# Performance work log

Measured on AMD Instinct MI355X. Metric: run time of the kernel, lower is better.

The kernel has to match this reference:

```python
import jax, jax.numpy as jnp
import numpy as np

DIM = 1024
HEADS = 16
DIM_HEAD = 64
INNER = HEADS * DIM_HEAD  # 1024
EPS = 1e-5


def layer_norm(x, g, b):
    mu = jnp.mean(x, axis=-1, keepdims=True)
    var = jnp.var(x, axis=-1, keepdims=True)
    return (x - mu) * jax.lax.rsqrt(var + EPS) * g + b


def setup_inputs() -> dict:
    key = jax.random.key(0)
    ks = jax.random.split(key, 8)
    s = 0.02
    return {
        "x": jax.random.normal(ks[0], (2, 2048, DIM), dtype=jnp.float32),
        "w_qkv": jax.random.normal(ks[1], (DIM, 3 * INNER), dtype=jnp.float32) * s,
        "w_out": jax.random.normal(ks[2], (INNER, DIM), dtype=jnp.float32) * s,
        "b_out": jnp.zeros((DIM,), jnp.float32),
        "g1": jnp.ones((DIM,), jnp.float32),
        "bt1": jnp.zeros((DIM,), jnp.float32),
        "g2": jnp.ones((DIM,), jnp.float32),
        "bt2": jnp.zeros((DIM,), jnp.float32),
        "w1": jax.random.normal(ks[3], (DIM, DIM), dtype=jnp.float32) * s,  # ff hidden = dim_out = DIM
        "b1": jnp.zeros((DIM,), jnp.float32),
        "w2": jax.random.normal(ks[4], (DIM, DIM), dtype=jnp.float32) * s,
        "b2": jnp.zeros((DIM,), jnp.float32),
    }


def reference(x, w_qkv, w_out, b_out, g1, bt1, g2, bt2, w1, b1, w2, b2):
    b, n, _ = x.shape
    scale = DIM_HEAD ** (-0.5)
    x_in = x
    xl = layer_norm(x, g1, bt1)
    qkv = xl @ w_qkv  # [b, n, 3*inner]
    q, k, v = jnp.split(qkv, 3, axis=-1)
    def split_heads(t):
        return t.reshape(b, n, HEADS, DIM_HEAD).transpose(0, 2, 1, 3)  # b h n d
    q, k, v = map(split_heads, (q, k, v))
    dots = jnp.einsum('bhid,bhjd->bhij', q, k) * scale
    attn = jax.nn.softmax(dots, axis=-1)
    out = jnp.einsum('bhij,bhjd->bhid', attn, v)
    out = out.transpose(0, 2, 1, 3).reshape(b, n, INNER)
    out = out @ w_out + b_out
    out = out + x_in
    h = layer_norm(out, g2, bt2)
    h = jax.nn.gelu(h @ w1 + b1, approximate=False) @ w2 + b2
    return h + out
```

## Files before the change

kernel.cpp:

```cpp
#include <hip/hip_runtime.h>
#include <math.h>

typedef __attribute__((ext_vector_type(4))) float f32x4;
typedef __attribute__((ext_vector_type(8))) short bf16x8;
typedef __attribute__((ext_vector_type(8))) unsigned short u16x8;

#define DIM 1024
#define SEQ 2048
#define NHEADS 16
#define DH 64

__device__ __forceinline__ unsigned short f2bf(float f) {
    unsigned int u = __builtin_bit_cast(unsigned int, f);
    u += 0x7fffu + ((u >> 16) & 1u);
    return (unsigned short)(u >> 16);
}

__device__ __forceinline__ float bf2f(unsigned short s) {
    unsigned int u = (unsigned int)s << 16;
    return __builtin_bit_cast(float, u);
}

__device__ __forceinline__ unsigned int cvt_pk_bf16(float lo, float hi) {
    unsigned int r;
    asm("v_cvt_pk_bf16_f32 %0, %1, %2" : "=v"(r) : "v"(lo), "v"(hi));
    return r;
}

__device__ __forceinline__ float fexp2(float x) {
    float r;
    asm("v_exp_f32 %0, %1" : "=v"(r) : "v"(x));
    return r;
}

__device__ __forceinline__ void gld16(const unsigned short* g, unsigned short* l) {
    __builtin_amdgcn_global_load_lds((const __attribute__((address_space(1))) void*)g,
                                     (__attribute__((address_space(3))) void*)l, 16, 0, 0);
}

__global__ __launch_bounds__(256) void wtrans_ln(const float* __restrict__ wq,
                                                 const float* __restrict__ wo,
                                                 const float* __restrict__ wf1,
                                                 const float* __restrict__ wf2,
                                                 unsigned short* __restrict__ oq,
                                                 unsigned short* __restrict__ oo,
                                                 unsigned short* __restrict__ of1,
                                                 unsigned short* __restrict__ of2, float sc,
                                                 const float* __restrict__ x,
                                                 const float* __restrict__ g1,
                                                 const float* __restrict__ bt1,
                                                 unsigned short* __restrict__ xl) {
    int z = blockIdx.z;
    int bxi = blockIdx.x;
    int tid = threadIdx.x;
    if (z == 4) {
        int row = blockIdx.y * 128 + bxi;
        const float4* xr = (const float4*)(x + (size_t)row * DIM);
        float4 v = xr[tid];
        float s1 = v.x + v.y + v.z + v.w;
        float s2 = v.x * v.x + v.y * v.y + v.z * v.z + v.w * v.w;
#pragma unroll
        for (int m = 32; m >= 1; m >>= 1) {
            s1 += __shfl_xor(s1, m);
            s2 += __shfl_xor(s2, m);
        }
        __shared__ float r1[4], r2[4];
        int w = tid >> 6;
        if ((tid & 63) == 0) { r1[w] = s1; r2[w] = s2; }
        __syncthreads();
        s1 = r1[0] + r1[1] + r1[2] + r1[3];
        s2 = r2[0] + r2[1] + r2[2] + r2[3];
        float mu = s1 * (1.0f / DIM);
        float var = s2 * (1.0f / DIM) - mu * mu;
        float rstd = rsqrtf(var + 1e-5f);
        float4 g4 = ((const float4*)g1)[tid];
        float4 b4 = ((const float4*)bt1)[tid];
        ushort4 ov;
        ov.x = f2bf((v.x - mu) * rstd * g4.x + b4.x);
        ov.y = f2bf((v.y - mu) * rstd * g4.y + b4.y);
        ov.z = f2bf((v.z - mu) * rstd * g4.z + b4.z);
        ov.w = f2bf((v.w - mu) * rstd * g4.w + b4.w);
        *(ushort4*)(xl + (size_t)row * DIM + tid * 4) = ov;
        return;
    }
    if (bxi >= (z == 0 ? 96 : 32)) return;
    const float* w = z == 0 ? wq : z == 1 ? wo : z == 2 ? wf1 : wf2;
    unsigned short* wt = z == 0 ? oq : z == 1 ? oo : z == 2 ? of1 : of2;
    int N = z == 0 ? 3072 : 1024;
    int scale_n = z == 0 ? 1024 : 0;
    const int K = 1024;
    __shared__ float t[32][33];
    int n0 = bxi * 32, k0 = blockIdx.y * 32;
    int c = tid & 31, rb = tid >> 5;
#pragma unroll
    for (int i = 0; i < 4; ++i) {
        int r = rb + i * 8;
        t[r][c] = w[(size_t)(k0 + r) * N + n0 + c];
    }
    __syncthreads();
#pragma unroll
    for (int i = 0; i < 4; ++i) {
        int r = rb + i * 8;
        float v = t[c][r];
        if (n0 + r < scale_n) v *= sc;
        wt[(size_t)(n0 + r) * K + k0 + c] = f2bf(v);
    }
}

__global__ __launch_bounds__(256) void ln_bf16(const unsigned short* __restrict__ x,
                                               const float* __restrict__ g,
                                               const float* __restrict__ bt,
                                               unsigned short* __restrict__ o) {
    int row = blockIdx.x, tid = threadIdx.x;
    ushort4 v4 = *(const ushort4*)(x + (size_t)row * DIM + tid * 4);
    float vx = bf2f(v4.x), vy = bf2f(v4.y), vz = bf2f(v4.z), vw = bf2f(v4.w);
    float s1 = vx + vy + vz + vw;
    float s2 = vx * vx + vy * vy + vz * vz + vw * vw;
#pragma unroll
    for (int m = 32; m >= 1; m >>= 1) {
        s1 += __shfl_xor(s1, m);
        s2 += __shfl_xor(s2, m);
    }
    __shared__ float r1[4], r2[4];
    int w = tid >> 6;
    if ((tid & 63) == 0) { r1[w] = s1; r2[w] = s2; }
    __syncthreads();
    s1 = r1[0] + r1[1] + r1[2] + r1[3];
    s2 = r2[0] + r2[1] + r2[2] + r2[3];
    float mu = s1 * (1.0f / DIM);
    float var = s2 * (1.0f / DIM) - mu * mu;
    float rstd = rsqrtf(var + 1e-5f);
    float4 g4 = ((const float4*)g)[tid];
    float4 b4 = ((const float4*)bt)[tid];
    ushort4 ov;
    ov.x = f2bf((vx - mu) * rstd * g4.x + b4.x);
    ov.y = f2bf((vy - mu) * rstd * g4.y + b4.y);
    ov.z = f2bf((vz - mu) * rstd * g4.z + b4.z);
    ov.w = f2bf((vw - mu) * rstd * g4.w + b4.w);
    *(ushort4*)(o + (size_t)row * DIM + tid * 4) = ov;
}

__global__ __launch_bounds__(512) void gemm256_qkv(const unsigned short* __restrict__ A,
                                                   const unsigned short* __restrict__ BT,
                                                   unsigned short* __restrict__ C,
                                                   unsigned short* __restrict__ vt,
                                                   int M, int N, int K, int nbx) {
    __shared__ unsigned short SM[65536];
    unsigned short* As = SM;
    unsigned short* Bs = SM + 32768;
    int tid = threadIdx.x;
    int lane = tid & 63, w = tid >> 6;
    int l15 = lane & 15, lhi = lane >> 4;
    int wr = w >> 2, wc = w & 3;
    int nwg = gridDim.x, wg = blockIdx.x;
    int swz = (wg & 7) * (nwg >> 3) + (wg >> 3);
    int bx = swz % nbx, by = swz / nbx;
    int row0 = by * 256, col0 = bx * 256;
    f32x4 zero = {0.f, 0.f, 0.f, 0.f};
    f32x4 acc[8][4];
#pragma unroll
    for (int i = 0; i < 8; ++i)
#pragma unroll
        for (int j = 0; j < 4; ++j) acc[i][j] = zero;
    auto stageA = [&](int slot, int kt) {
#pragma unroll
        for (int p = 0; p < 4; ++p) {
            int u = tid + p * 512;
            int r = u >> 3, cu = u & 7;
            int scu = cu ^ (r & 7);
            gld16(A + (size_t)(row0 + r) * K + kt * 64 + scu * 8, As + slot * 16384 + u * 8);
        }
    };
    auto stageB = [&](int slot, int kt) {
#pragma unroll
        for (int p = 0; p < 4; ++p) {
            int u = tid + p * 512;
            int r = u >> 3, cu = u & 7;
            int scu = cu ^ (r & 7);
            gld16(BT + (size_t)(col0 + r) * K + kt * 64 + scu * 8, Bs + slot * 16384 + u * 8);
        }
    };
    int nk = K / 64;
    stageB(0, 0);
    stageA(0, 0);
    stageB(1, 1);
    stageA(1, 1);
    asm volatile("s_waitcnt vmcnt(8)" ::: "memory");
    __builtin_amdgcn_s_barrier();
    __builtin_amdgcn_sched_barrier(0);
    for (int t = 0; t < nk; ++t) {
        int cur = t & 1;
        const unsigned short* Ab = As + cur * 16384;
        const unsigned short* Bb = Bs + cur * 16384;
        bf16x8 bfr[4][2];
#pragma unroll
        for (int j = 0; j < 4; ++j)
#pragma unroll
            for (int kk = 0; kk < 2; ++kk) {
                int rr = wc * 64 + j * 16 + l15;
                bfr[j][kk] = *(const bf16x8*)&Bb[rr * 64 + (((kk * 4 + lhi) ^ (rr & 7)) * 8)];
            }
#pragma unroll
        for (int q = 0; q < 4; ++q) {
            bf16x8 af[2][2];
#pragma unroll
            for (int i2 = 0; i2 < 2; ++i2)
#pragma unroll
                for (int kk = 0; kk < 2; ++kk) {
                    int rr = wr * 128 + (q * 2 + i2) * 16 + l15;
                    af[i2][kk] = *(const bf16x8*)&Ab[rr * 64 + (((kk * 4 + lhi) ^ (rr & 7)) * 8)];
                }
#pragma unroll
            for (int kk = 0; kk < 2; ++kk)
#pragma unroll
                for (int i2 = 0; i2 < 2; ++i2)
#pragma unroll
                    for (int j = 0; j < 4; ++j)
                        acc[q * 2 + i2][j] = __builtin_amdgcn_mfma_f32_16x16x32_bf16(
                            af[i2][kk], bfr[j][kk], acc[q * 2 + i2][j], 0, 0, 0);
            if (q == 0) {
                __builtin_amdgcn_sched_barrier(0);
                __builtin_amdgcn_s_barrier();
                __builtin_amdgcn_sched_barrier(0);
                if (t + 2 < nk) stageB(cur, t + 2);
            }
        }
        __builtin_amdgcn_sched_barrier(0);
        __builtin_amdgcn_s_barrier();
        __builtin_amdgcn_sched_barrier(0);
        if (t + 2 < nk) stageA(cur, t + 2);
        if (t + 1 < nk) {
            if (t + 2 < nk)
                asm volatile("s_waitcnt vmcnt(8)" ::: "memory");
            else
                asm volatile("s_waitcnt vmcnt(0)" ::: "memory");
            __builtin_amdgcn_s_barrier();
            __builtin_amdgcn_sched_barrier(0);
        }
    }
    if (col0 >= 2048) {
        __builtin_amdgcn_sched_barrier(0);
        __syncthreads();
        unsigned short* Ct = SM;
#pragma unroll
        for (int i = 0; i < 8; ++i)
#pragma unroll
            for (int j = 0; j < 4; ++j)
#pragma unroll
                for (int r = 0; r < 4; ++r) {
                    int row = wr * 128 + i * 16 + lhi * 4 + r;
                    int col = wc * 64 + j * 16 + l15;
                    Ct[row * 256 + (col ^ (((row >> 2) & 7) << 3))] = f2bf(acc[i][j][r]);
                }
        __syncthreads();
        int b = row0 >> 11, n0 = row0 & 2047;
        int h0 = (col0 - 2048) >> 6;
        int c = tid >> 1, hf = tid & 1;
        int hl = c >> 6, d = c & 63;
        unsigned short* vrow =
            vt + ((size_t)(b * NHEADS + h0 + hl) * DH + d) * SEQ + n0 + hf * 128;
#pragma unroll
        for (int s8 = 0; s8 < 16; ++s8) {
            u16x8 val;
#pragma unroll
            for (int j = 0; j < 8; ++j) {
                int nn = hf * 128 + s8 * 8 + j;
                int ntl = nn >> 6, s = nn & 63;
                int sig = (s & 32) | ((s & 4) << 2) | ((s & 24) >> 1) | (s & 3);
                int rr = ntl * 64 + sig;
                val[j] = Ct[rr * 256 + (c ^ (((rr >> 2) & 7) << 3))];
            }
            *(u16x8*)(vrow + s8 * 8) = val;
        }
        return;
    }
#pragma unroll
    for (int i = 0; i < 8; ++i)
#pragma unroll
        for (int j = 0; j < 4; ++j)
#pragma unroll
            for (int r = 0; r < 4; ++r) {
                int row = row0 + wr * 128 + i * 16 + lhi * 4 + r;
                int col = col0 + wc * 64 + j * 16 + l15;
                C[(size_t)row * N + col] = f2bf(acc[i][j][r]);
            }
}

template <int BN, int BK, int OBF, int BIAS, int GELU_, int RESID>
__global__ __launch_bounds__(256) void gemm_kernel(const unsigned short* __restrict__ A,
                                                   const unsigned short* __restrict__ BT,
                                                   void* __restrict__ C,
                                                   const float* __restrict__ bias,
                                                   const void* __restrict__ resid,
                                                   int M, int N, int K, int nbx) {
    constexpr int U = BK / 8;
    constexpr int NAU = 128 * U;
    constexpr int NBU = BN * U;
    constexpr int PT = (NAU + NBU) / 256;
    constexpr int NJ = BN / 32;
    constexpr int KK = BK / 32;
    extern __shared__ char smem[];
    unsigned short* As = (unsigned short*)smem;
    unsigned short* Bs = As + 3 * 128 * BK;
    int tid = threadIdx.x;
    int lane = tid & 63, w = tid >> 6;
    int l15 = lane & 15, lhi = lane >> 4;
    int nwg = gridDim.x, wg = blockIdx.x;
    int swz = (wg & 7) * (nwg >> 3) + (wg >> 3);
    int bx = swz % nbx, by = swz / nbx;
    int row0 = by * 128, col0 = bx * BN;
    int wrow = (w >> 1) * 64, wcol = (w & 1) * (16 * NJ);
    auto rh = [](int rr) -> int {
        if constexpr (U == 4) return (rr ^ (rr >> 2)) & 3;
        else return rr & (U - 1);
    };
    f32x4 zero = {0.f, 0.f, 0.f, 0.f};
    f32x4 acc[4][NJ];
#pragma unroll
    for (int i = 0; i < 4; ++i)
#pragma unroll
        for (int j = 0; j < NJ; ++j) acc[i][j] = zero;
    auto stage = [&](int buf, int kt) {
#pragma unroll
        for (int p = 0; p < PT; ++p) {
            if (p * 256 < NAU) {
                int u = tid + p * 256;
                int r = u / U, cu = u % U;
                int scu = cu ^ rh(r);
                gld16(A + (size_t)(row0 + r) * K + kt * BK + scu * 8, As + buf * 128 * BK + u * 8);
            } else {
                int ub = tid + p * 256 - NAU;
                int r = ub / U, cu = ub % U;
                int scu = cu ^ rh(r);
                gld16(BT + (size_t)(col0 + r) * K + kt * BK + scu * 8, Bs + buf * BN * BK + ub * 8);
            }
        }
    };
    int nk = K / BK;
    stage(0, 0);
    stage(1, 1);
    asm volatile("s_waitcnt vmcnt(%0)" ::"i"(PT) : "memory");
    __builtin_amdgcn_s_barrier();
    __builtin_amdgcn_sched_barrier(0);
    int cur = 0;
    for (int kt = 0; kt < nk; ++kt) {
        int nxt2 = cur + 2 >= 3 ? cur - 1 : cur + 2;
        if (kt + 2 < nk) stage(nxt2, kt + 2);
        const unsigned short* Ab = As + cur * 128 * BK;
        const unsigned short* Bb = Bs + cur * BN * BK;
        bf16x8 af[4][KK], bfr[NJ][KK];
#pragma unroll
        for (int i = 0; i < 4; ++i)
#pragma unroll
            for (int kk = 0; kk < KK; ++kk) {
                int rr = wrow + i * 16 + l15;
                int up = (kk * 4 + lhi) ^ rh(rr);
                af[i][kk] = *(const bf16x8*)&Ab[rr * BK + up * 8];
            }
#pragma unroll
        for (int j = 0; j < NJ; ++j)
#pragma unroll
            for (int kk = 0; kk < KK; ++kk) {
                int rr = wcol + j * 16 + l15;
                int up = (kk * 4 + lhi) ^ rh(rr);
                bfr[j][kk] = *(const bf16x8*)&Bb[rr * BK + up * 8];
            }
#pragma unroll
        for (int kk = 0; kk < KK; ++kk)
#pragma unroll
            for (int i = 0; i < 4; ++i)
#pragma unroll
                for (int j = 0; j < NJ; ++j)
                    acc[i][j] = __builtin_amdgcn_mfma_f32_16x16x32_bf16(af[i][kk], bfr[j][kk],
                                                                        acc[i][j], 0, 0, 0);
        __builtin_amdgcn_sched_barrier(0);
        if (kt + 1 < nk) {
            if (kt + 2 < nk)
                asm volatile("s_waitcnt vmcnt(%0)" ::"i"(PT) : "memory");
            else
                asm volatile("s_waitcnt vmcnt(0)" ::: "memory");
            __builtin_amdgcn_s_barrier();
            __builtin_amdgcn_sched_barrier(0);
        }
        cur = cur + 1 == 3 ? 0 : cur + 1;
    }
#pragma unroll
    for (int i = 0; i < 4; ++i)
#pragma unroll
        for (int j = 0; j < NJ; ++j)
#pragma unroll
            for (int r = 0; r < 4; ++r) {
                int row = row0 + wrow + i * 16 + lhi * 4 + r;
                int col = col0 + wcol + j * 16 + l15;
                float v = acc[i][j][r];
                if (BIAS) v += bias[col];
                if (GELU_) v = 0.5f * v * (1.0f + erff(v * 0.70710678118f));
                if (RESID == 1) v += ((const float*)resid)[(size_t)row * N + col];
                if (RESID == 2) v += bf2f(((const unsigned short*)resid)[(size_t)row * N + col]);
                if (OBF)
                    ((unsigned short*)C)[(size_t)row * N + col] = f2bf(v);
                else
                    ((float*)C)[(size_t)row * N + col] = v;
            }
}

__global__ __launch_bounds__(256) void attn_kernel(const unsigned short* __restrict__ qkv,
                                                   const unsigned short* __restrict__ vt,
                                                   unsigned short* __restrict__ o) {
    __shared__ unsigned short Ks[2][64 * 64];
    __shared__ unsigned short Vs[2][64 * 64];
    int tid = threadIdx.x;
    int lane = tid & 63, w = tid >> 6;
    int l15 = lane & 15, lhi = lane >> 4;
    int wg = blockIdx.x;
    int swz = (wg & 7) * 128 + (wg >> 3);
    int qt = swz & 31, h = (swz >> 5) & 15, b = swz >> 9;
    const unsigned short* qb =
        qkv + (size_t)(b * SEQ + qt * 64 + w * 16 + l15) * 3072 + h * DH;
    bf16x8 qf0 = *(const bf16x8*)(qb + lhi * 8);
    bf16x8 qf1 = *(const bf16x8*)(qb + 32 + lhi * 8);
    f32x4 zero = {0.f, 0.f, 0.f, 0.f};
    f32x4 oacc[4], lacc = zero;
#pragma unroll
    for (int i = 0; i < 4; ++i) oacc[i] = zero;
    const short one_s = (short)0x3F80;
    bf16x8 ones = {one_s, one_s, one_s, one_s, one_s, one_s, one_s, one_s};
    int srow = tid >> 3;
    int scx = (tid & 7) ^ (srow & 7);
    const unsigned short* kb = qkv + (size_t)b * SEQ * 3072 + 1024 + h * DH;
    const unsigned short* vb = vt + (size_t)(b * NHEADS + h) * DH * SEQ;
    const unsigned short* k0 = kb + (size_t)srow * 3072 + scx * 8;
    const unsigned short* v0 = vb + (size_t)srow * SEQ + scx * 8;
    auto stage = [&](int buf, int kt) {
        unsigned short* lk = &Ks[buf][0] + tid * 8;
        unsigned short* lv = &Vs[buf][0] + tid * 8;
        gld16(k0 + (size_t)kt * 64 * 3072, lk);
        gld16(k0 + ((size_t)kt * 64 + 32) * 3072, lk + 2048);
        gld16(v0 + kt * 64, lv);
        gld16(v0 + (size_t)32 * SEQ + kt * 64, lv + 2048);
    };
    const int NT = SEQ / 64;
    stage(0, 0);
    asm volatile("s_waitcnt vmcnt(0)" ::: "memory");
    __builtin_amdgcn_s_barrier();
    __builtin_amdgcn_sched_barrier(0);
    int kx = l15 & 7;
    for (int kt = 0; kt < NT; ++kt) {
        int cur = kt & 1;
        if (kt + 1 < NT) stage(cur ^ 1, kt + 1);
        const unsigned short* Kc = &Ks[cur][0];
        const unsigned short* Vc = &Vs[cur][0];
        f32x4 sacc[4];
#pragma unroll
        for (int nt = 0; nt < 4; ++nt) {
            bf16x8 kf0 = *(const bf16x8*)&Kc[(nt * 16 + l15) * 64 + ((lhi ^ kx) * 8)];
            bf16x8 kf1 = *(const bf16x8*)&Kc[(nt * 16 + l15) * 64 + (((4 + lhi) ^ kx) * 8)];
            f32x4 z = __builtin_amdgcn_mfma_f32_16x16x32_bf16(kf0, qf0, zero, 0, 0, 0);
            sacc[nt] = __builtin_amdgcn_mfma_f32_16x16x32_bf16(kf1, qf1, z, 0, 0, 0);
        }
        bf16x8 pf[2];
#pragma unroll
        for (int kc = 0; kc < 2; ++kc) {
            union { bf16x8 v; unsigned int u[4]; } pu;
            pu.u[0] = cvt_pk_bf16(fexp2(sacc[2 * kc][0]), fexp2(sacc[2 * kc][1]));
            pu.u[1] = cvt_pk_bf16(fexp2(sacc[2 * kc][2]), fexp2(sacc[2 * kc][3]));
            pu.u[2] = cvt_pk_bf16(fexp2(sacc[2 * kc + 1][0]), fexp2(sacc[2 * kc + 1][1]));
            pu.u[3] = cvt_pk_bf16(fexp2(sacc[2 * kc + 1][2]), fexp2(sacc[2 * kc + 1][3]));
            pf[kc] = pu.v;
        }
#pragma unroll
        for (int dt = 0; dt < 4; ++dt)
#pragma unroll
            for (int kc = 0; kc < 2; ++kc) {
                bf16x8 vf = *(const bf16x8*)&Vc[(dt * 16 + l15) * 64 + (((kc * 4 + lhi) ^ kx) * 8)];
                oacc[dt] = __builtin_amdgcn_mfma_f32_16x16x32_bf16(vf, pf[kc], oacc[dt], 0, 0, 0);
            }
        lacc = __builtin_amdgcn_mfma_f32_16x16x32_bf16(ones, pf[0], lacc, 0, 0, 0);
        lacc = __builtin_amdgcn_mfma_f32_16x16x32_bf16(ones, pf[1], lacc, 0, 0, 0);
        __builtin_amdgcn_sched_barrier(0);
        if (kt + 1 < NT) {
            asm volatile("s_waitcnt vmcnt(0)" ::: "memory");
            __builtin_amdgcn_s_barrier();
            __builtin_amdgcn_sched_barrier(0);
        }
    }
    float rl = 1.0f / lacc[0];
    size_t orow = (size_t)(b * SEQ + qt * 64 + w * 16 + l15) * DIM + h * DH;
#pragma unroll
    for (int dt = 0; dt < 4; ++dt) {
        ushort4 st;
        st.x = f2bf(oacc[dt][0] * rl);
        st.y = f2bf(oacc[dt][1] * rl);
        st.z = f2bf(oacc[dt][2] * rl);
        st.w = f2bf(oacc[dt][3] * rl);
        *(ushort4*)(o + orow + dt * 16 + lhi * 4) = st;
    }
}

extern "C" void kernel_launch(void* const* d_in, const int* in_sizes, int n_in,
                              void* d_out, int out_size, void* d_ws, size_t ws_size,
                              hipStream_t stream) {
    (void)in_sizes; (void)n_in; (void)out_size; (void)ws_size;
    const float* x = (const float*)d_in[0];
    const float* w_qkv = (const float*)d_in[1];
    const float* w_out = (const float*)d_in[2];
    const float* b_out = (const float*)d_in[3];
    const float* g1 = (const float*)d_in[4];
    const float* bt1 = (const float*)d_in[5];
    const float* g2 = (const float*)d_in[6];
    const float* bt2 = (const float*)d_in[7];
    const float* w1 = (const float*)d_in[8];
    const float* b1 = (const float*)d_in[9];
    const float* w2 = (const float*)d_in[10];
    const float* b2 = (const float*)d_in[11];
    float* out = (float*)d_out;

    char* ws = (char*)d_ws;
    size_t off = 0;
    auto alloc = [&](size_t bytes) {
        void* p = ws + off;
        off += (bytes + 255) & ~(size_t)255;
        return p;
    };
    const int R = 2 * SEQ;
    unsigned short* xl    = (unsigned short*)alloc((size_t)R * DIM * 2);
    unsigned short* wqkvT = (unsigned short*)alloc((size_t)3 * DIM * DIM * 2);
    unsigned short* woutT = (unsigned short*)alloc((size_t)DIM * DIM * 2);
    unsigned short* w1T   = (unsigned short*)alloc((size_t)DIM * DIM * 2);
    unsigned short* w2T   = (unsigned short*)alloc((size_t)DIM * DIM * 2);
    unsigned short* qkvb  = (unsigned short*)alloc((size_t)R * 3 * DIM * 2);
    unsigned short* vtb   = (unsigned short*)alloc((size_t)R * DIM * 2);
    unsigned short* attO  = (unsigned short*)alloc((size_t)R * DIM * 2);
    unsigned short* outb  = (unsigned short*)alloc((size_t)R * DIM * 2);
    unsigned short* h2    = (unsigned short*)alloc((size_t)R * DIM * 2);
    unsigned short* ffn1  = (unsigned short*)alloc((size_t)R * DIM * 2);

    const float CS = 0.125f * 1.44269504f;
    wtrans_ln<<<dim3(128, 32, 5), 256, 0, stream>>>(w_qkv, w_out, w1, w2, wqkvT, woutT, w1T, w2T,
                                                    CS, x, g1, bt1, xl);

    const unsigned int SH_FFN = (3 * 128 * 64 + 3 * 64 * 64) * 2;
    gemm256_qkv<<<dim3((R / 256) * (3 * DIM / 256)), 512, 0, stream>>>(
        xl, wqkvT, qkvb, vtb, R, 3 * DIM, DIM, 3 * DIM / 256);
    attn_kernel<<<2 * NHEADS * (SEQ / 64), 256, 0, stream>>>(qkvb, vtb, attO);
    gemm_kernel<64, 64, 1, 1, 0, 1><<<dim3((DIM / 64) * (R / 128)), 256, SH_FFN, stream>>>(
        attO, woutT, outb, b_out, x, R, DIM, DIM, DIM / 64);
    ln_bf16<<<R, 256, 0, stream>>>(outb, g2, bt2, h2);
    gemm_kernel<64, 64, 1, 1, 1, 0><<<dim3((DIM / 64) * (R / 128)), 256, SH_FFN, stream>>>(
        h2, w1T, ffn1, b1, nullptr, R, DIM, DIM, DIM / 64);
    gemm_kernel<64, 64, 0, 1, 0, 2><<<dim3((DIM / 64) * (R / 128)), 256, SH_FFN, stream>>>(
        ffn1, w2T, out, b2, outb, R, DIM, DIM, DIM / 64);
}
```

Before: 155.3 us.

## Split attention over KV quarters with 128-row Q tiles and add combine kernel

The attention kernel now handles 128 query rows per block, two 16-row groups per wave, so each K/V tile in shared memory is reused twice as often. The key sequence is split into four quarters across separate blocks (split-K), each writing unnormalized bf16 partial outputs and row sums, and a new combine kernel adds the partials and normalizes. Double buffering of K/V is dropped in favour of a single buffer with load, wait, then compute. The change trades more grid parallelism and fewer LDS loads per MFMA for extra global traffic on partial outputs, an extra launch, bf16 rounding of partials and no load/compute overlap.

```diff
diff --git a/kernel.cpp b/kernel.cpp
--- a/kernel.cpp
+++ b/kernel.cpp
@@ -406,23 +406,32 @@
 
 __global__ __launch_bounds__(256) void attn_kernel(const unsigned short* __restrict__ qkv,
                                                    const unsigned short* __restrict__ vt,
-                                                   unsigned short* __restrict__ o) {
-    __shared__ unsigned short Ks[2][64 * 64];
-    __shared__ unsigned short Vs[2][64 * 64];
+                                                   unsigned short* __restrict__ po,
+                                                   float* __restrict__ pl) {
+    __shared__ unsigned short Ks[64 * 64];
+    __shared__ unsigned short Vs[64 * 64];
     int tid = threadIdx.x;
     int lane = tid & 63, w = tid >> 6;
     int l15 = lane & 15, lhi = lane >> 4;
     int wg = blockIdx.x;
-    int swz = (wg & 7) * 128 + (wg >> 3);
-    int qt = swz & 31, h = (swz >> 5) & 15, b = swz >> 9;
-    const unsigned short* qb =
-        qkv + (size_t)(b * SEQ + qt * 64 + w * 16 + l15) * 3072 + h * DH;
-    bf16x8 qf0 = *(const bf16x8*)(qb + lhi * 8);
-    bf16x8 qf1 = *(const bf16x8*)(qb + 32 + lhi * 8);
+    int swz = (wg & 7) * 256 + (wg >> 3);
+    int qt = swz & 15, quarter = (swz >> 4) & 3, h = (swz >> 6) & 15, b = swz >> 10;
+    bf16x8 qf[2][2];
+#pragma unroll
+    for (int qg = 0; qg < 2; ++qg) {
+        const unsigned short* qb =
+            qkv + (size_t)(b * SEQ + qt * 128 + w * 32 + qg * 16 + l15) * 3072 + h * DH;
+        qf[qg][0] = *(const bf16x8*)(qb + lhi * 8);
+        qf[qg][1] = *(const bf16x8*)(qb + 32 + lhi * 8);
+    }
     f32x4 zero = {0.f, 0.f, 0.f, 0.f};
-    f32x4 oacc[4], lacc = zero;
-#pragma unroll
-    for (int i = 0; i < 4; ++i) oacc[i] = zero;
+    f32x4 oacc[2][4], lacc[2];
+#pragma unroll
+    for (int qg = 0; qg < 2; ++qg) {
+        lacc[qg] = zero;
+#pragma unroll
+        for (int i = 0; i < 4; ++i) oacc[qg][i] = zero;
+    }
     const short one_s = (short)0x3F80;
     bf16x8 ones = {one_s, one_s, one_s, one_s, one_s, one_s, one_s, one_s};
     int srow = tid >> 3;
@@ -431,70 +440,104 @@
     const unsigned short* vb = vt + (size_t)(b * NHEADS + h) * DH * SEQ;
     const unsigned short* k0 = kb + (size_t)srow * 3072 + scx * 8;
     const unsigned short* v0 = vb + (size_t)srow * SEQ + scx * 8;
-    auto stage = [&](int buf, int kt) {
-        unsigned short* lk = &Ks[buf][0] + tid * 8;
-        unsigned short* lv = &Vs[buf][0] + tid * 8;
-        gld16(k0 + (size_t)kt * 64 * 3072, lk);
-        gld16(k0 + ((size_t)kt * 64 + 32) * 3072, lk + 2048);
-        gld16(v0 + kt * 64, lv);
-        gld16(v0 + (size_t)32 * SEQ + kt * 64, lv + 2048);
+    auto stage = [&](int kg) {
+        unsigned short* lk = &Ks[0] + tid * 8;
+        unsigned short* lv = &Vs[0] + tid * 8;
+        gld16(k0 + (size_t)kg * 64 * 3072, lk);
+        gld16(k0 + ((size_t)kg * 64 + 32) * 3072, lk + 2048);
+        gld16(v0 + kg * 64, lv);
+        gld16(v0 + (size_t)32 * SEQ + kg * 64, lv + 2048);
     };
-    const int NT = SEQ / 64;
-    stage(0, 0);
-    asm volatile("s_waitcnt vmcnt(0)" ::: "memory");
-    __builtin_amdgcn_s_barrier();
-    __builtin_amdgcn_sched_barrier(0);
     int kx = l15 & 7;
-    for (int kt = 0; kt < NT; ++kt) {
-        int cur = kt & 1;
-        if (kt + 1 < NT) stage(cur ^ 1, kt + 1);
-        const unsigned short* Kc = &Ks[cur][0];
-        const unsigned short* Vc = &Vs[cur][0];
-        f32x4 sacc[4];
+    const int NT4 = SEQ / 64 / 4;
+    for (int kt = 0; kt < NT4; ++kt) {
+        stage(quarter * NT4 + kt);
+        asm volatile("s_waitcnt vmcnt(0)" ::: "memory");
+        __builtin_amdgcn_s_barrier();
+        __builtin_amdgcn_sched_barrier(0);
+        f32x4 sacc[2][4];
 #pragma unroll
         for (int nt = 0; nt < 4; ++nt) {
-            bf16x8 kf0 = *(const bf16x8*)&Kc[(nt * 16 + l15) * 64 + ((lhi ^ kx) * 8)];
-            bf16x8 kf1 = *(const bf16x8*)&Kc[(nt * 16 + l15) * 64 + (((4 + lhi) ^ kx) * 8)];
-            f32x4 z = __builtin_amdgcn_mfma_f32_16x16x32_bf16(kf0, qf0, zero, 0, 0, 0);
-            sacc[nt] = __builtin_amdgcn_mfma_f32_16x16x32_bf16(kf1, qf1, z, 0, 0, 0);
-        }
-        bf16x8 pf[2];
-#pragma unroll
-        for (int kc = 0; kc < 2; ++kc) {
-            union { bf16x8 v; unsigned int u[4]; } pu;
-            pu.u[0] = cvt_pk_bf16(fexp2(sacc[2 * kc][0]), fexp2(sacc[2 * kc][1]));
-            pu.u[1] = cvt_pk_bf16(fexp2(sacc[2 * kc][2]), fexp2(sacc[2 * kc][3]));
-            pu.u[2] = cvt_pk_bf16(fexp2(sacc[2 * kc + 1][0]), fexp2(sacc[2 * kc + 1][1]));
-            pu.u[3] = cvt_pk_bf16(fexp2(sacc[2 * kc + 1][2]), fexp2(sacc[2 * kc + 1][3]));
-            pf[kc] = pu.v;
-        }
+            bf16x8 kf0 = *(const bf16x8*)&Ks[(nt * 16 + l15) * 64 + ((lhi ^ kx) * 8)];
+            bf16x8 kf1 = *(const bf16x8*)&Ks[(nt * 16 + l15) * 64 + (((4 + lhi) ^ kx) * 8)];
+#pragma unroll
+            for (int qg = 0; qg < 2; ++qg) {
+                f32x4 z = __builtin_amdgcn_mfma_f32_16x16x32_bf16(kf0, qf[qg][0], zero, 0, 0, 0);
+                sacc[qg][nt] = __builtin_amdgcn_mfma_f32_16x16x32_bf16(kf1, qf[qg][1], z, 0, 0, 0);
+            }
+        }
+        bf16x8 pf[2][2];
+#pragma unroll
+        for (int qg = 0; qg < 2; ++qg)
+#pragma unroll
+            for (int kc = 0; kc < 2; ++kc) {
+                union { bf16x8 v; unsigned int u[4]; } pu;
+                pu.u[0] = cvt_pk_bf16(fexp2(sacc[qg][2 * kc][0]), fexp2(sacc[qg][2 * kc][1]));
+                pu.u[1] = cvt_pk_bf16(fexp2(sacc[qg][2 * kc][2]), fexp2(sacc[qg][2 * kc][3]));
+                pu.u[2] = cvt_pk_bf16(fexp2(sacc[qg][2 * kc + 1][0]), fexp2(sacc[qg][2 * kc + 1][1]));
+                pu.u[3] = cvt_pk_bf16(fexp2(sacc[qg][2 * kc + 1][2]), fexp2(sacc[qg][2 * kc + 1][3]));
+                pf[qg][kc] = pu.v;
+            }
 #pragma unroll
         for (int dt = 0; dt < 4; ++dt)
 #pragma unroll
             for (int kc = 0; kc < 2; ++kc) {
-                bf16x8 vf = *(const bf16x8*)&Vc[(dt * 16 + l15) * 64 + (((kc * 4 + lhi) ^ kx) * 8)];
-                oacc[dt] = __builtin_amdgcn_mfma_f32_16x16x32_bf16(vf, pf[kc], oacc[dt], 0, 0, 0);
-            }
-        lacc = __builtin_amdgcn_mfma_f32_16x16x32_bf16(ones, pf[0], lacc, 0, 0, 0);
-        lacc = __builtin_amdgcn_mfma_f32_16x16x32_bf16(ones, pf[1], lacc, 0, 0, 0);
+                bf16x8 vf = *(const bf16x8*)&Vs[(dt * 16 + l15) * 64 + (((kc * 4 + lhi) ^ kx) * 8)];
+#pragma unroll
+                for (int qg = 0; qg < 2; ++qg)
+                    oacc[qg][dt] =
+                        __builtin_amdgcn_mfma_f32_16x16x32_bf16(vf, pf[qg][kc], oacc[qg][dt], 0, 0, 0);
+            }
+#pragma unroll
+        for (int qg = 0; qg < 2; ++qg) {
+            lacc[qg] = __builtin_amdgcn_mfma_f32_16x16x32_bf16(ones, pf[qg][0], lacc[qg], 0, 0, 0);
+            lacc[qg] = __builtin_amdgcn_mfma_f32_16x16x32_bf16(ones, pf[qg][1], lacc[qg], 0, 0, 0);
+        }
         __builtin_amdgcn_sched_barrier(0);
-        if (kt + 1 < NT) {
-            asm volatile("s_waitcnt vmcnt(0)" ::: "memory");
+        if (kt + 1 < NT4) {
             __builtin_amdgcn_s_barrier();
             __builtin_amdgcn_sched_barrier(0);
         }
     }
-    float rl = 1.0f / lacc[0];
-    size_t orow = (size_t)(b * SEQ + qt * 64 + w * 16 + l15) * DIM + h * DH;
-#pragma unroll
-    for (int dt = 0; dt < 4; ++dt) {
-        ushort4 st;
-        st.x = f2bf(oacc[dt][0] * rl);
-        st.y = f2bf(oacc[dt][1] * rl);
-        st.z = f2bf(oacc[dt][2] * rl);
-        st.w = f2bf(oacc[dt][3] * rl);
-        *(ushort4*)(o + orow + dt * 16 + lhi * 4) = st;
-    }
+#pragma unroll
+    for (int qg = 0; qg < 2; ++qg) {
+        int rrow = b * SEQ + qt * 128 + w * 32 + qg * 16 + l15;
+        unsigned short* pob = po + ((size_t)quarter * 4096 + rrow) * DIM + h * DH;
+#pragma unroll
+        for (int dt = 0; dt < 4; ++dt) {
+            ushort4 st;
+            st.x = f2bf(oacc[qg][dt][0]);
+            st.y = f2bf(oacc[qg][dt][1]);
+            st.z = f2bf(oacc[qg][dt][2]);
+            st.w = f2bf(oacc[qg][dt][3]);
+            *(ushort4*)(pob + dt * 16 + lhi * 4) = st;
+        }
+        if (lhi == 0) pl[((size_t)quarter * 4096 + rrow) * NHEADS + h] = lacc[qg][0];
+    }
+}
+
+__global__ __launch_bounds__(256) void attn_combine(const unsigned short* __restrict__ po,
+                                                    const float* __restrict__ pl,
+                                                    unsigned short* __restrict__ o) {
+    int r = blockIdx.x, tid = threadIdx.x;
+    int d0 = tid * 4, h = d0 >> 6;
+    float sx = 0.f, sy = 0.f, sz = 0.f, sw = 0.f, sl = 0.f;
+#pragma unroll
+    for (int q = 0; q < 4; ++q) {
+        ushort4 a = *(const ushort4*)(po + (size_t)(q * 4096 + r) * DIM + d0);
+        sx += bf2f(a.x);
+        sy += bf2f(a.y);
+        sz += bf2f(a.z);
+        sw += bf2f(a.w);
+        sl += pl[(size_t)(q * 4096 + r) * NHEADS + h];
+    }
+    float rl = 1.0f / sl;
+    ushort4 ov;
+    ov.x = f2bf(sx * rl);
+    ov.y = f2bf(sy * rl);
+    ov.z = f2bf(sz * rl);
+    ov.w = f2bf(sw * rl);
+    *(ushort4*)(o + (size_t)r * DIM + d0) = ov;
 }
 
 extern "C" void kernel_launch(void* const* d_in, const int* in_sizes, int n_in,
@@ -534,6 +577,8 @@
     unsigned short* outb  = (unsigned short*)alloc((size_t)R * DIM * 2);
     unsigned short* h2    = (unsigned short*)alloc((size_t)R * DIM * 2);
     unsigned short* ffn1  = (unsigned short*)alloc((size_t)R * DIM * 2);
+    unsigned short* po = (unsigned short*)alloc((size_t)4 * R * DIM * 2);
+    float* pl = (float*)alloc((size_t)4 * R * NHEADS * 4);
 
     const float CS = 0.125f * 1.44269504f;
     wtrans_ln<<<dim3(128, 32, 5), 256, 0, stream>>>(w_qkv, w_out, w1, w2, wqkvT, woutT, w1T, w2T,
@@ -542,7 +587,8 @@
     const unsigned int SH_FFN = (3 * 128 * 64 + 3 * 64 * 64) * 2;
     gemm256_qkv<<<dim3((R / 256) * (3 * DIM / 256)), 512, 0, stream>>>(
         xl, wqkvT, qkvb, vtb, R, 3 * DIM, DIM, 3 * DIM / 256);
-    attn_kernel<<<2 * NHEADS * (SEQ / 64), 256, 0, stream>>>(qkvb, vtb, attO);
+    attn_kernel<<<2 * NHEADS * (SEQ / 128) * 4, 256, 0, stream>>>(qkvb, vtb, po, pl);
+    attn_combine<<<R, 256, 0, stream>>>(po, pl, attO);
     gemm_kernel<64, 64, 1, 1, 0, 1><<<dim3((DIM / 64) * (R / 128)), 256, SH_FFN, stream>>>(
         attO, woutT, outb, b_out, x, R, DIM, DIM, DIM / 64);
     ln_bf16<<<R, 256, 0, stream>>>(outb, g2, bt2, h2);
```

New measurement: 162.4 us. 4.6% more time.
